# Kernel optimization log

Hardware: AMD Instinct MI355X
Metric: run time of the kernel (lower is better)

Reference implementation:

```python
import jax, jax.numpy as jnp
import numpy as np

B, DS, DM = 4, 64, 4096
NE, S = 1024, 2048


def setup_inputs() -> dict:
    key = jax.random.key(0)
    ks = jax.random.split(key, 9)
    std = 0.02
    return {
        "state": jax.random.normal(ks[0], (B, DS, DM), jnp.float32),
        "evicted_tokens": jax.random.normal(ks[1], (B, NE, DM), jnp.float32),
        "current_tokens": jax.random.normal(ks[2], (B, S, DM), jnp.float32),
        "W_key": std * jax.random.normal(ks[3], (DS, DM), jnp.float32),
        "W_beta_w": std * jax.random.normal(ks[4], (DS, DM), jnp.float32),
        "W_beta_b": jnp.zeros((DS,), jnp.float32),
        "W_query": std * jax.random.normal(ks[5], (DS, DM), jnp.float32),
        "gate_w": std * jax.random.normal(ks[6], (1, DM), jnp.float32),
        "gate_b": jnp.full((1,), -2.0, jnp.float32),  # gate_bias init
    }


def reference(state, evicted_tokens, current_tokens, W_key, W_beta_w, W_beta_b,
              W_query, gate_w, gate_b):
    # ---- compress: fold evicted tokens into SSM state ----
    # keys: [B, NE, DS]; softmax over the token axis (dim=1)
    keys = jnp.einsum('bnd,sd->bns', evicted_tokens, W_key)
    write_weights = jax.nn.softmax(keys, axis=1)
    # update: [B, DS, DM] = write_weights^T @ evicted_tokens
    update = jnp.einsum('bns,bnd->bsd', write_weights, evicted_tokens)
    summary = evicted_tokens.mean(axis=1)  # [B, DM]
    beta = jax.nn.sigmoid(summary @ W_beta_w.T + W_beta_b)  # [B, DS]
    new_state = beta[:, :, None] * state + update  # [B, DS, DM]
    # ---- query: gated linear-attention readout ----
    q = jnp.einsum('bld,sd->bls', current_tokens, W_query)  # [B, S, DS]
    retrieved = jnp.einsum('bls,bsd->bld', q, new_state)    # [B, S, DM]
    gate = jax.nn.sigmoid(current_tokens @ gate_w.T + gate_b)  # [B, S, 1]
    return gate * retrieved
```

## Files before the change

kernel.cpp:

```cpp
#include <hip/hip_runtime.h>

#define DM 4096
#define DSZ 64
#define NE 1024
#define SQ 2048
#define NB 4

typedef __attribute__((ext_vector_type(8))) short bf16x8;
typedef __attribute__((ext_vector_type(4))) float f32x4;

__device__ __forceinline__ unsigned f2bf(float f) {
  union { float f; unsigned u; } v; v.f = f;
  return (v.u + 0x7fffu + ((v.u >> 16) & 1u)) >> 16;
}
__device__ __forceinline__ unsigned pack2(float lo, float hi) {
  return f2bf(lo) | (f2bf(hi) << 16);
}
__device__ __forceinline__ float bf2f(unsigned short h) {
  union { unsigned u; float f; } v; v.u = ((unsigned)h) << 16; return v.f;
}

__device__ __forceinline__ void load8(const float* __restrict__ ap, const float* __restrict__ bp,
                                      float4& a0, float4& a1, float4& a2, float4& a3,
                                      float4& b0, float4& b1, float4& b2, float4& b3) {
  a0 = *(const float4*)(ap);      a1 = *(const float4*)(ap + 4);
  a2 = *(const float4*)(ap + 8);  a3 = *(const float4*)(ap + 12);
  b0 = *(const float4*)(bp);      b1 = *(const float4*)(bp + 4);
  b2 = *(const float4*)(bp + 8);  b3 = *(const float4*)(bp + 12);
}

__launch_bounds__(256)
__global__ void k_keys(const float* __restrict__ ev, const float* __restrict__ Wk,
                       float* __restrict__ keys_part, unsigned short* __restrict__ evb,
                       float* __restrict__ summary) {
  __shared__ __align__(16) unsigned short As[2][64][72];
  __shared__ __align__(16) unsigned short Bs[2][64][72];
  __shared__ float csum[8][4][64];
  const int bid = blockIdx.x;
  const int ks = bid & 7, mt = (bid >> 3) & 15, b = bid >> 7;
  const int n0 = mt * 64;
  const int t = threadIdx.x;
  const int w = t >> 6, m15 = t & 15, quad = (t & 63) >> 4;
  const int rowS = t >> 2, seg = (t & 3) * 16;
  const int ccol = t & 63, cgrp = t >> 6;

  f32x4 acc[4];
#pragma unroll
  for (int i = 0; i < 4; ++i) acc[i] = (f32x4){0.f, 0.f, 0.f, 0.f};

  const float* ap = ev + ((size_t)(b * NE + n0 + rowS)) * DM + ks * 512 + seg;
  const float* bp = Wk + (size_t)rowS * DM + ks * 512 + seg;
  unsigned short* evp = evb + ((size_t)(b * NE + n0 + rowS)) * DM + ks * 512 + seg;

  float4 a0, a1, a2, a3, b0, b1, b2, b3;
  load8(ap, bp, a0, a1, a2, a3, b0, b1, b2, b3);
  int cur = 0;
  for (int ch = 0; ch < 8; ++ch) {
    uint4 pa0 = { pack2(a0.x,a0.y), pack2(a0.z,a0.w), pack2(a1.x,a1.y), pack2(a1.z,a1.w) };
    uint4 pa1 = { pack2(a2.x,a2.y), pack2(a2.z,a2.w), pack2(a3.x,a3.y), pack2(a3.z,a3.w) };
    *(uint4*)&As[cur][rowS][seg]     = pa0;
    *(uint4*)&As[cur][rowS][seg + 8] = pa1;
    *(uint4*)&Bs[cur][rowS][seg]     = (uint4){ pack2(b0.x,b0.y), pack2(b0.z,b0.w), pack2(b1.x,b1.y), pack2(b1.z,b1.w) };
    *(uint4*)&Bs[cur][rowS][seg + 8] = (uint4){ pack2(b2.x,b2.y), pack2(b2.z,b2.w), pack2(b3.x,b3.y), pack2(b3.z,b3.w) };
    *(uint4*)(evp)     = pa0;
    *(uint4*)(evp + 8) = pa1;
    __syncthreads();
    if (ch < 7) {
      ap += 64; bp += 64; evp += 64;
      load8(ap, bp, a0, a1, a2, a3, b0, b1, b2, b3);
    }
    {
      float cs = 0.f;
#pragma unroll
      for (int r = 0; r < 16; ++r) cs += bf2f(As[cur][cgrp * 16 + r][ccol]);
      csum[ch][cgrp][ccol] = cs;
    }
#pragma unroll
    for (int kk = 0; kk < 2; ++kk) {
      bf16x8 af = *(const bf16x8*)&As[cur][w * 16 + m15][kk * 32 + quad * 8];
#pragma unroll
      for (int tn = 0; tn < 4; ++tn) {
        bf16x8 bfr = *(const bf16x8*)&Bs[cur][tn * 16 + m15][kk * 32 + quad * 8];
        acc[tn] = __builtin_amdgcn_mfma_f32_16x16x32_bf16(af, bfr, acc[tn], 0, 0, 0);
      }
    }
    cur ^= 1;
  }
  const int n = n0 + w * 16 + quad * 4;
#pragma unroll
  for (int tn = 0; tn < 4; ++tn) {
    const int s = tn * 16 + m15;
    float4 v = { acc[tn][0], acc[tn][1], acc[tn][2], acc[tn][3] };
    *(float4*)&keys_part[(size_t)ks * (NB * DSZ * NE) + ((size_t)(b * DSZ + s)) * NE + n] = v;
  }
  __syncthreads();
  if (t < 64) {
#pragma unroll
    for (int c2 = 0; c2 < 8; ++c2) {
      float ssum = csum[c2][0][t] + csum[c2][1][t] + csum[c2][2][t] + csum[c2][3][t];
      atomicAdd(&summary[b * DM + ks * 512 + c2 * 64 + t], ssum * (1.f / 1024.f));
    }
  }
}

__launch_bounds__(256)
__global__ void k_bs(const float* __restrict__ summary, const float* __restrict__ Wbw,
                     const float* __restrict__ Wbb, const float* __restrict__ keys_part,
                     float* __restrict__ beta, unsigned short* __restrict__ ww_t) {
  __shared__ float wredb[4];
  __shared__ float wred[8];
  const int b = blockIdx.x >> 6, s = blockIdx.x & 63;
  const int t = threadIdx.x;
  {
    const float* sp = summary + b * DM + t * 16;
    const float* wp = Wbw + (size_t)s * DM + t * 16;
    float acc = 0.f;
#pragma unroll
    for (int j = 0; j < 4; ++j) {
      float4 a  = *(const float4*)(sp + j * 4);
      float4 w4 = *(const float4*)(wp + j * 4);
      acc += a.x * w4.x + a.y * w4.y + a.z * w4.z + a.w * w4.w;
    }
#pragma unroll
    for (int off = 32; off > 0; off >>= 1) acc += __shfl_xor(acc, off);
    if ((t & 63) == 0) wredb[t >> 6] = acc;
  }
  const size_t base = ((size_t)(b * DSZ + s)) * NE + t * 4;
  float4 k = {0.f, 0.f, 0.f, 0.f};
#pragma unroll
  for (int sl = 0; sl < 8; ++sl) {
    float4 p = *(const float4*)&keys_part[(size_t)sl * (NB * DSZ * NE) + base];
    k.x += p.x; k.y += p.y; k.z += p.z; k.w += p.w;
  }
  float m = fmaxf(fmaxf(k.x, k.y), fmaxf(k.z, k.w));
#pragma unroll
  for (int off = 32; off > 0; off >>= 1) m = fmaxf(m, __shfl_xor(m, off));
  if ((t & 63) == 0) wred[t >> 6] = m;
  __syncthreads();
  const float M = fmaxf(fmaxf(wred[0], wred[1]), fmaxf(wred[2], wred[3]));
  float4 e = { expf(k.x - M), expf(k.y - M), expf(k.z - M), expf(k.w - M) };
  float ss = e.x + e.y + e.z + e.w;
#pragma unroll
  for (int off = 32; off > 0; off >>= 1) ss += __shfl_xor(ss, off);
  if ((t & 63) == 0) wred[4 + (t >> 6)] = ss;
  __syncthreads();
  const float inv = 1.f / (wred[4] + wred[5] + wred[6] + wred[7]);
  ushort4 o = { (unsigned short)f2bf(e.x * inv), (unsigned short)f2bf(e.y * inv),
                (unsigned short)f2bf(e.z * inv), (unsigned short)f2bf(e.w * inv) };
  *(ushort4*)&ww_t[((size_t)(b * DSZ + s)) * NE + t * 4] = o;
  if (t == 0) {
    float x = wredb[0] + wredb[1] + wredb[2] + wredb[3] + Wbb[s];
    beta[b * DSZ + s] = 1.f / (1.f + expf(-x));
  }
}

__launch_bounds__(256)
__global__ void k_update(const unsigned short* __restrict__ evb, const float* __restrict__ state,
                         const float* __restrict__ beta, const unsigned short* __restrict__ ww_t,
                         unsigned short* __restrict__ ns_t) {
  __shared__ __align__(16) unsigned short Aw[2][64][72];
  __shared__ __align__(16) unsigned short Bt[2][32][72];
  const int bid = blockIdx.x;
  const int dt = bid & 127, b = bid >> 7;
  const int d0 = dt * 32;
  const int t = threadIdx.x;
  const int w = t >> 6, m15 = t & 15, quad = (t & 63) >> 4;
  const int rowS = t >> 2, seg = (t & 3) * 16;
  const int npair = (t & 31) * 2, dquad = (t >> 5) * 4;

  f32x4 acc[2];
#pragma unroll
  for (int i = 0; i < 2; ++i) acc[i] = (f32x4){0.f, 0.f, 0.f, 0.f};

  const unsigned short* wp = ww_t + ((size_t)(b * DSZ + rowS)) * NE + seg;
  const unsigned short* ep = evb + ((size_t)(b * NE + npair)) * DM + d0 + dquad;

  uint4 wa = *(const uint4*)(wp), wb = *(const uint4*)(wp + 8);
  uint2 r0 = *(const uint2*)(ep), r1 = *(const uint2*)(ep + DM);
  int cur = 0;
  for (int ch = 0; ch < 16; ++ch) {
    *(uint4*)&Aw[cur][rowS][seg]     = wa;
    *(uint4*)&Aw[cur][rowS][seg + 8] = wb;
    *(unsigned*)&Bt[cur][dquad + 0][npair] = (r0.x & 0xffffu) | (r1.x << 16);
    *(unsigned*)&Bt[cur][dquad + 1][npair] = (r0.x >> 16) | (r1.x & 0xffff0000u);
    *(unsigned*)&Bt[cur][dquad + 2][npair] = (r0.y & 0xffffu) | (r1.y << 16);
    *(unsigned*)&Bt[cur][dquad + 3][npair] = (r0.y >> 16) | (r1.y & 0xffff0000u);
    __syncthreads();
    if (ch < 15) {
      wp += 64; ep += (size_t)64 * DM;
      wa = *(const uint4*)(wp); wb = *(const uint4*)(wp + 8);
      r0 = *(const uint2*)(ep); r1 = *(const uint2*)(ep + DM);
    }
#pragma unroll
    for (int kk = 0; kk < 2; ++kk) {
      bf16x8 af = *(const bf16x8*)&Aw[cur][w * 16 + m15][kk * 32 + quad * 8];
#pragma unroll
      for (int tn = 0; tn < 2; ++tn) {
        bf16x8 bfr = *(const bf16x8*)&Bt[cur][tn * 16 + m15][kk * 32 + quad * 8];
        acc[tn] = __builtin_amdgcn_mfma_f32_16x16x32_bf16(af, bfr, acc[tn], 0, 0, 0);
      }
    }
    cur ^= 1;
  }
  const int sbase = w * 16 + quad * 4;
#pragma unroll
  for (int tn = 0; tn < 2; ++tn) {
    const int d = d0 + tn * 16 + m15;
    float v[4];
#pragma unroll
    for (int r = 0; r < 4; ++r) {
      const int s = sbase + r;
      v[r] = beta[b * DSZ + s] * state[((size_t)(b * DSZ + s)) * DM + d] + acc[tn][r];
    }
    ushort4 o = { (unsigned short)f2bf(v[0]), (unsigned short)f2bf(v[1]),
                  (unsigned short)f2bf(v[2]), (unsigned short)f2bf(v[3]) };
    *(ushort4*)&ns_t[((size_t)(b * DM + d)) * DSZ + sbase] = o;
  }
}

__launch_bounds__(256)
__global__ void k_q(const float* __restrict__ cur_, const float* __restrict__ Wq,
                    const float* __restrict__ gate_w,
                    float* __restrict__ q_part, float* __restrict__ gate_acc) {
  __shared__ __align__(16) unsigned short As[2][64][72];
  __shared__ __align__(16) unsigned short Bs[2][64][72];
  __shared__ float gwAll[1024];
  __shared__ float gred[256];
  const int bid = blockIdx.x;
  const int ks = bid & 3, mt = (bid >> 2) & 31, b = bid >> 7;
  const int l0 = mt * 64;
  const int t = threadIdx.x;
  const int w = t >> 6, m15 = t & 15, quad = (t & 63) >> 4;
  const int rowS = t >> 2, seg = (t & 3) * 16;

  f32x4 acc[4];
#pragma unroll
  for (int i = 0; i < 4; ++i) acc[i] = (f32x4){0.f, 0.f, 0.f, 0.f};
  float gpart = 0.f;

  *(float4*)&gwAll[t * 4] = *(const float4*)(gate_w + ks * 1024 + t * 4);

  const float* ap = cur_ + ((size_t)(b * SQ + l0 + rowS)) * DM + ks * 1024 + seg;
  const float* bp = Wq + (size_t)rowS * DM + ks * 1024 + seg;

  float4 a0, a1, a2, a3, b0, b1, b2, b3;
  load8(ap, bp, a0, a1, a2, a3, b0, b1, b2, b3);
  int cur = 0;
  for (int ch = 0; ch < 16; ++ch) {
    *(uint4*)&As[cur][rowS][seg]     = (uint4){ pack2(a0.x,a0.y), pack2(a0.z,a0.w), pack2(a1.x,a1.y), pack2(a1.z,a1.w) };
    *(uint4*)&As[cur][rowS][seg + 8] = (uint4){ pack2(a2.x,a2.y), pack2(a2.z,a2.w), pack2(a3.x,a3.y), pack2(a3.z,a3.w) };
    *(uint4*)&Bs[cur][rowS][seg]     = (uint4){ pack2(b0.x,b0.y), pack2(b0.z,b0.w), pack2(b1.x,b1.y), pack2(b1.z,b1.w) };
    *(uint4*)&Bs[cur][rowS][seg + 8] = (uint4){ pack2(b2.x,b2.y), pack2(b2.z,b2.w), pack2(b3.x,b3.y), pack2(b3.z,b3.w) };
    __syncthreads();
    {
      const float* g = &gwAll[ch * 64 + seg];
      gpart += a0.x*g[0]  + a0.y*g[1]  + a0.z*g[2]  + a0.w*g[3]
             + a1.x*g[4]  + a1.y*g[5]  + a1.z*g[6]  + a1.w*g[7]
             + a2.x*g[8]  + a2.y*g[9]  + a2.z*g[10] + a2.w*g[11]
             + a3.x*g[12] + a3.y*g[13] + a3.z*g[14] + a3.w*g[15];
    }
    if (ch < 15) {
      ap += 64; bp += 64;
      load8(ap, bp, a0, a1, a2, a3, b0, b1, b2, b3);
    }
#pragma unroll
    for (int kk = 0; kk < 2; ++kk) {
      bf16x8 af = *(const bf16x8*)&As[cur][w * 16 + m15][kk * 32 + quad * 8];
#pragma unroll
      for (int tn = 0; tn < 4; ++tn) {
        bf16x8 bfr = *(const bf16x8*)&Bs[cur][tn * 16 + m15][kk * 32 + quad * 8];
        acc[tn] = __builtin_amdgcn_mfma_f32_16x16x32_bf16(af, bfr, acc[tn], 0, 0, 0);
      }
    }
    cur ^= 1;
  }
  const int lrow = l0 + w * 16 + quad * 4;
#pragma unroll
  for (int tn = 0; tn < 4; ++tn) {
#pragma unroll
    for (int r = 0; r < 4; ++r) {
      q_part[(size_t)ks * (NB * SQ * DSZ) + ((size_t)(b * SQ + lrow + r)) * DSZ + tn * 16 + m15] =
          acc[tn][r];
    }
  }
  gred[t] = gpart;
  __syncthreads();
  if (t < 64) {
    float tot = gred[4 * t] + gred[4 * t + 1] + gred[4 * t + 2] + gred[4 * t + 3];
    atomicAdd(&gate_acc[b * SQ + l0 + t], tot);
  }
}

__launch_bounds__(256)
__global__ void k_out(const float* __restrict__ q_part, const unsigned short* __restrict__ ns_t,
                      const float* __restrict__ gate_acc, const float* __restrict__ gate_b,
                      float* __restrict__ out) {
  __shared__ __align__(16) unsigned short Qs[64][72];
  const int bid = blockIdx.x;
  const int dt = bid & 63, lt = (bid >> 6) & 31, b = bid >> 11;
  const int d0 = dt * 64, l0 = lt * 64;
  const int t = threadIdx.x;
  const int w = t >> 6, m15 = t & 15, quad = (t & 63) >> 4;
  const int rowS = t >> 2, seg = (t & 3) * 16;
  {
    const int SL = NB * SQ * DSZ;
    const float* qp = q_part + ((size_t)(b * SQ + l0 + rowS)) * DSZ + seg;
    float4 s0 = {0,0,0,0}, s1 = s0, s2 = s0, s3 = s0;
#pragma unroll
    for (int sl = 0; sl < 4; ++sl) {
      const float* p = qp + (size_t)sl * SL;
      float4 u0 = *(const float4*)(p);
      float4 u1 = *(const float4*)(p + 4);
      float4 u2 = *(const float4*)(p + 8);
      float4 u3 = *(const float4*)(p + 12);
      s0.x += u0.x; s0.y += u0.y; s0.z += u0.z; s0.w += u0.w;
      s1.x += u1.x; s1.y += u1.y; s1.z += u1.z; s1.w += u1.w;
      s2.x += u2.x; s2.y += u2.y; s2.z += u2.z; s2.w += u2.w;
      s3.x += u3.x; s3.y += u3.y; s3.z += u3.z; s3.w += u3.w;
    }
    *(uint4*)&Qs[rowS][seg]     = (uint4){ pack2(s0.x,s0.y), pack2(s0.z,s0.w), pack2(s1.x,s1.y), pack2(s1.z,s1.w) };
    *(uint4*)&Qs[rowS][seg + 8] = (uint4){ pack2(s2.x,s2.y), pack2(s2.z,s2.w), pack2(s3.x,s3.y), pack2(s3.z,s3.w) };
  }
  __syncthreads();
  f32x4 acc[4];
#pragma unroll
  for (int i = 0; i < 4; ++i) acc[i] = (f32x4){0.f, 0.f, 0.f, 0.f};
#pragma unroll
  for (int kk = 0; kk < 2; ++kk) {
    bf16x8 af = *(const bf16x8*)&Qs[w * 16 + m15][kk * 32 + quad * 8];
#pragma unroll
    for (int tn = 0; tn < 4; ++tn) {
      const int d = d0 + tn * 16 + m15;
      bf16x8 bfr = *(const bf16x8*)&ns_t[((size_t)(b * DM + d)) * DSZ + kk * 32 + quad * 8];
      acc[tn] = __builtin_amdgcn_mfma_f32_16x16x32_bf16(af, bfr, acc[tn], 0, 0, 0);
    }
  }
  const float gb = gate_b[0];
  const int lbase = l0 + w * 16 + quad * 4;
  float g[4];
#pragma unroll
  for (int r = 0; r < 4; ++r)
    g[r] = 1.f / (1.f + expf(-(gate_acc[b * SQ + lbase + r] + gb)));
#pragma unroll
  for (int tn = 0; tn < 4; ++tn) {
    const int d = d0 + tn * 16 + m15;
#pragma unroll
    for (int r = 0; r < 4; ++r)
      out[((size_t)(b * SQ + lbase + r)) * DM + d] = g[r] * acc[tn][r];
  }
}

extern "C" void kernel_launch(void* const* d_in, const int* in_sizes, int n_in,
                              void* d_out, int out_size, void* d_ws, size_t ws_size,
                              hipStream_t stream) {
  const float* state   = (const float*)d_in[0];
  const float* evicted = (const float*)d_in[1];
  const float* current = (const float*)d_in[2];
  const float* Wkey    = (const float*)d_in[3];
  const float* Wbw     = (const float*)d_in[4];
  const float* Wbb     = (const float*)d_in[5];
  const float* Wq      = (const float*)d_in[6];
  const float* gate_w  = (const float*)d_in[7];
  const float* gate_b  = (const float*)d_in[8];
  float* out = (float*)d_out;

  float* f = (float*)d_ws;
  float* keys_part = f;
  float* q_part    = keys_part + 8 * 262144;
  float* summary   = q_part + 4 * 524288;
  float* gate_acc  = summary + 16384;
  float* beta      = gate_acc + 8192;
  unsigned short* ww_t = (unsigned short*)(beta + 256);
  unsigned short* ns_t = ww_t + 262144;
  unsigned short* evb  = ns_t + 1048576;

  hipMemsetAsync(summary, 0, (16384 + 8192) * sizeof(float), stream);

  k_keys   <<<512,  256, 0, stream>>>(evicted, Wkey, keys_part, evb, summary);
  k_q      <<<512,  256, 0, stream>>>(current, Wq, gate_w, q_part, gate_acc);
  k_bs     <<<256,  256, 0, stream>>>(summary, Wbw, Wbb, keys_part, beta, ww_t);
  k_update <<<512,  256, 0, stream>>>(evb, state, beta, ww_t, ns_t);
  k_out    <<<8192, 256, 0, stream>>>(q_part, ns_t, gate_acc, gate_b, out);
}
```

Before: 391.7 us.

## Transpose MFMA operands for vectorized stores and widen k_out tiles to reuse Q

```diff
diff --git a/kernel.cpp b/kernel.cpp
--- a/kernel.cpp
+++ b/kernel.cpp
@@ -265,23 +265,22 @@
     }
 #pragma unroll
     for (int kk = 0; kk < 2; ++kk) {
-      bf16x8 af = *(const bf16x8*)&As[cur][w * 16 + m15][kk * 32 + quad * 8];
+      bf16x8 af = *(const bf16x8*)&Bs[cur][w * 16 + m15][kk * 32 + quad * 8];
 #pragma unroll
       for (int tn = 0; tn < 4; ++tn) {
-        bf16x8 bfr = *(const bf16x8*)&Bs[cur][tn * 16 + m15][kk * 32 + quad * 8];
+        bf16x8 bfr = *(const bf16x8*)&As[cur][tn * 16 + m15][kk * 32 + quad * 8];
         acc[tn] = __builtin_amdgcn_mfma_f32_16x16x32_bf16(af, bfr, acc[tn], 0, 0, 0);
       }
     }
     cur ^= 1;
   }
-  const int lrow = l0 + w * 16 + quad * 4;
+  const int srow = w * 16 + quad * 4;
+  const int SL = NB * SQ * DSZ;
 #pragma unroll
   for (int tn = 0; tn < 4; ++tn) {
-#pragma unroll
-    for (int r = 0; r < 4; ++r) {
-      q_part[(size_t)ks * (NB * SQ * DSZ) + ((size_t)(b * SQ + lrow + r)) * DSZ + tn * 16 + m15] =
-          acc[tn][r];
-    }
+    const int l = l0 + tn * 16 + m15;
+    float4 v = { acc[tn][0], acc[tn][1], acc[tn][2], acc[tn][3] };
+    *(float4*)&q_part[(size_t)ks * SL + ((size_t)(b * SQ + l)) * DSZ + srow] = v;
   }
   gred[t] = gpart;
   __syncthreads();
@@ -297,8 +296,8 @@
                       float* __restrict__ out) {
   __shared__ __align__(16) unsigned short Qs[64][72];
   const int bid = blockIdx.x;
-  const int dt = bid & 63, lt = (bid >> 6) & 31, b = bid >> 11;
-  const int d0 = dt * 64, l0 = lt * 64;
+  const int dseg = bid & 15, lt = (bid >> 4) & 31, b = bid >> 9;
+  const int dbase = dseg * 256, l0 = lt * 64;
   const int t = threadIdx.x;
   const int w = t >> 6, m15 = t & 15, quad = (t & 63) >> 4;
   const int rowS = t >> 2, seg = (t & 3) * 16;
@@ -321,32 +320,35 @@
     *(uint4*)&Qs[rowS][seg]     = (uint4){ pack2(s0.x,s0.y), pack2(s0.z,s0.w), pack2(s1.x,s1.y), pack2(s1.z,s1.w) };
     *(uint4*)&Qs[rowS][seg + 8] = (uint4){ pack2(s2.x,s2.y), pack2(s2.z,s2.w), pack2(s3.x,s3.y), pack2(s3.z,s3.w) };
   }
-  __syncthreads();
-  f32x4 acc[4];
-#pragma unroll
-  for (int i = 0; i < 4; ++i) acc[i] = (f32x4){0.f, 0.f, 0.f, 0.f};
-#pragma unroll
-  for (int kk = 0; kk < 2; ++kk) {
-    bf16x8 af = *(const bf16x8*)&Qs[w * 16 + m15][kk * 32 + quad * 8];
+  const float gb = gate_b[0];
+  float g[4];
+#pragma unroll
+  for (int tn = 0; tn < 4; ++tn)
+    g[tn] = 1.f / (1.f + expf(-(gate_acc[b * SQ + l0 + tn * 16 + m15] + gb)));
+  __syncthreads();
+  for (int dsub = 0; dsub < 4; ++dsub) {
+    const int d0 = dbase + dsub * 64;
+    const int drow = d0 + w * 16 + m15;
+    f32x4 acc[4];
+#pragma unroll
+    for (int i = 0; i < 4; ++i) acc[i] = (f32x4){0.f, 0.f, 0.f, 0.f};
+#pragma unroll
+    for (int kk = 0; kk < 2; ++kk) {
+      bf16x8 af = *(const bf16x8*)&ns_t[((size_t)(b * DM + drow)) * DSZ + kk * 32 + quad * 8];
+#pragma unroll
+      for (int tn = 0; tn < 4; ++tn) {
+        bf16x8 bfr = *(const bf16x8*)&Qs[tn * 16 + m15][kk * 32 + quad * 8];
+        acc[tn] = __builtin_amdgcn_mfma_f32_16x16x32_bf16(af, bfr, acc[tn], 0, 0, 0);
+      }
+    }
+    const int dcol = d0 + w * 16 + quad * 4;
 #pragma unroll
     for (int tn = 0; tn < 4; ++tn) {
-      const int d = d0 + tn * 16 + m15;
-      bf16x8 bfr = *(const bf16x8*)&ns_t[((size_t)(b * DM + d)) * DSZ + kk * 32 + quad * 8];
-      acc[tn] = __builtin_amdgcn_mfma_f32_16x16x32_bf16(af, bfr, acc[tn], 0, 0, 0);
-    }
-  }
-  const float gb = gate_b[0];
-  const int lbase = l0 + w * 16 + quad * 4;
-  float g[4];
-#pragma unroll
-  for (int r = 0; r < 4; ++r)
-    g[r] = 1.f / (1.f + expf(-(gate_acc[b * SQ + lbase + r] + gb)));
-#pragma unroll
-  for (int tn = 0; tn < 4; ++tn) {
-    const int d = d0 + tn * 16 + m15;
-#pragma unroll
-    for (int r = 0; r < 4; ++r)
-      out[((size_t)(b * SQ + lbase + r)) * DM + d] = g[r] * acc[tn][r];
+      const int l = l0 + tn * 16 + m15;
+      float4 v = { g[tn] * acc[tn][0], g[tn] * acc[tn][1],
+                   g[tn] * acc[tn][2], g[tn] * acc[tn][3] };
+      *(float4*)&out[((size_t)(b * SQ + l)) * DM + dcol] = v;
+    }
   }
 }
 
@@ -380,5 +382,5 @@
   k_q      <<<512,  256, 0, stream>>>(current, Wq, gate_w, q_part, gate_acc);
   k_bs     <<<256,  256, 0, stream>>>(summary, Wbw, Wbb, keys_part, beta, ww_t);
   k_update <<<512,  256, 0, stream>>>(evb, state, beta, ww_t, ns_t);
-  k_out    <<<8192, 256, 0, stream>>>(q_part, ns_t, gate_acc, gate_b, out);
-}
+  k_out    <<<2048, 256, 0, stream>>>(q_part, ns_t, gate_acc, gate_b, out);
+}
```

After: 354.1 us. -9.6%, faster.
